# Kernel optimization log

Measured on AMD Instinct MI355X. Metric: run time of the kernel, lower is better.

## Reference

```python
import jax, jax.numpy as jnp
import numpy as np

EMBED_DIM = 2048
NUM_HEADS = 16
HEAD_DIM = EMBED_DIM // NUM_HEADS


def setup_inputs() -> dict:
    key = jax.random.key(0)
    k_x, k_qkv, k_out = jax.random.split(key, 3)
    x = jax.random.normal(k_x, (4, 2048, EMBED_DIM), dtype=jnp.float32)
    # torch nn.Linear(in, out) weight is [out, in]; y = x @ W.T
    scale = 1.0 / np.sqrt(EMBED_DIM)
    W_qkv = jax.random.uniform(k_qkv, (3 * EMBED_DIM, EMBED_DIM), dtype=jnp.float32, minval=-scale, maxval=scale)
    W_out = jax.random.uniform(k_out, (EMBED_DIM, EMBED_DIM), dtype=jnp.float32, minval=-scale, maxval=scale)
    return {"x": x, "W_qkv": W_qkv, "W_out": W_out}


def reference(x, W_qkv, W_out):
    B, T, C = x.shape
    H, D = NUM_HEADS, HEAD_DIM
    qkv = jnp.einsum("btc,fc->btf", x, W_qkv)  # [B,T,3C]
    q, k, v = jnp.split(qkv, 3, axis=-1)
    q = q.reshape(B, T, H, D).transpose(0, 2, 1, 3)  # [B,H,T,D]
    k = k.reshape(B, T, H, D).transpose(0, 2, 1, 3)
    v = v.reshape(B, T, H, D).transpose(0, 2, 1, 3)
    att = jnp.einsum("bhqd,bhkd->bhqk", q, k) / jnp.sqrt(jnp.float32(D))
    causal = jnp.tril(jnp.ones((T, T), dtype=bool))
    att = jnp.where(causal[None, None], att, -jnp.inf)
    att = jax.nn.softmax(att, axis=-1)
    out = jnp.einsum("bhqk,bhkd->bhqd", att, v)  # [B,H,T,D]
    out = out.transpose(0, 2, 1, 3).reshape(B, T, C)
    return jnp.einsum("btc,oc->bto", out, W_out)
```

## Files before the change

kernel.cpp:

```cpp
#include <hip/hip_runtime.h>
#include <hip/hip_bf16.h>
#include <math.h>

#define BDIM 4
#define TDIM 2048
#define CDIM 2048
#define HDIM 16
#define DDIM 128
#define MROWS (BDIM*TDIM)
#define NQKV (3*CDIM)
#define GK   CDIM
#define QSZ  (MROWS*CDIM)

#define NTILES 32
#define NITER  16
#define HT     8192
#define BOFF   32768

#define QSCALE 0.1275171f

typedef __attribute__((ext_vector_type(8))) short short8;
typedef __attribute__((ext_vector_type(4))) unsigned short ushort4v;
typedef __attribute__((ext_vector_type(4))) float f32x4;

__device__ __forceinline__ unsigned short f2bf(float f) {
    unsigned int u = __float_as_uint(f);
    u += 0x7fffu + ((u >> 16) & 1u);
    return (unsigned short)(u >> 16);
}

__device__ __forceinline__ void gload16(const unsigned short* g, unsigned short* l) {
    __builtin_amdgcn_global_load_lds((__attribute__((address_space(1))) void*)(g),
                                     (__attribute__((address_space(3))) void*)(l),
                                     16, 0, 0);
}

__global__ __launch_bounds__(256) void cvt_all(const float* __restrict__ x,
                                               const float* __restrict__ wqkv,
                                               const float* __restrict__ wout,
                                               unsigned short* __restrict__ xb,
                                               unsigned short* __restrict__ wqkvb,
                                               unsigned short* __restrict__ woutb)
{
    const int stride = gridDim.x * blockDim.x;
    const int t0 = blockIdx.x * blockDim.x + threadIdx.x;
    for (int i = t0; i < MROWS*CDIM/4; i += stride) {
        float4 f = ((const float4*)x)[i];
        ushort4v u;
        u[0]=f2bf(f.x); u[1]=f2bf(f.y); u[2]=f2bf(f.z); u[3]=f2bf(f.w);
        ((ushort4v*)xb)[i] = u;
    }
    for (int i = t0; i < NQKV*CDIM/4; i += stride) {
        float4 f = ((const float4*)wqkv)[i];
        const float s = (i < CDIM*CDIM/4) ? QSCALE : 1.0f;
        ushort4v u;
        u[0]=f2bf(f.x*s); u[1]=f2bf(f.y*s); u[2]=f2bf(f.z*s); u[3]=f2bf(f.w*s);
        ((ushort4v*)wqkvb)[i] = u;
    }
    for (int i = t0; i < CDIM*CDIM/4; i += stride) {
        float4 f = ((const float4*)wout)[i];
        ushort4v u;
        u[0]=f2bf(f.x); u[1]=f2bf(f.y); u[2]=f2bf(f.z); u[3]=f2bf(f.w);
        ((ushort4v*)woutb)[i] = u;
    }
}

__device__ __forceinline__ void stage_half(const unsigned short* __restrict__ T,
                                           int rowbase, int kcol,
                                           unsigned short* dst, int w, int lane)
{
    const int sw = ((lane & 3) ^ ((lane >> 3) & 3)) * 8;
#pragma unroll
    for (int j = 0; j < 2; ++j) {
        const int r = w*32 + j*16 + (lane >> 2);
        gload16(T + (size_t)(rowbase + r)*GK + kcol + sw, dst + (w*32 + j*16)*32);
    }
}

template<int MQ, int KS, int BUF, bool RDB, bool WAIT>
__device__ __forceinline__ void gphase(unsigned short* lds,
    const unsigned short* __restrict__ stT, int stRow, int stKcol, unsigned short* stDst,
    int wr, int wc, int fr, int colu, int w, int lane,
    short8 (&bfr)[4], f32x4 (&acc)[8][4])
{
    const unsigned short* Ah = lds + (BUF*2 + KS)*HT;
    const unsigned short* Bh = lds + BOFF + (BUF*2 + KS)*HT;
    short8 af[4];
#pragma unroll
    for (int mi = 0; mi < 4; ++mi)
        af[mi] = *(const short8*)&Ah[(wr*128 + (MQ*4 + mi)*16 + fr)*32 + colu];
    if (RDB) {
#pragma unroll
        for (int nj = 0; nj < 4; ++nj)
            bfr[nj] = *(const short8*)&Bh[(wc*64 + nj*16 + fr)*32 + colu];
    }
    stage_half(stT, stRow, stKcol, stDst, w, lane);
    if (WAIT) asm volatile("s_waitcnt vmcnt(4)" ::: "memory");
    __builtin_amdgcn_s_barrier();
    asm volatile("s_waitcnt lgkmcnt(0)" ::: "memory");
    __builtin_amdgcn_sched_barrier(0);
    __builtin_amdgcn_s_setprio(1);
#pragma unroll
    for (int mi = 0; mi < 4; ++mi)
#pragma unroll
        for (int nj = 0; nj < 4; ++nj)
            acc[MQ*4 + mi][nj] = __builtin_amdgcn_mfma_f32_16x16x32_bf16(af[mi], bfr[nj], acc[MQ*4 + mi][nj], 0, 0, 0);
    __builtin_amdgcn_s_setprio(0);
    __builtin_amdgcn_s_barrier();
}

template<int MODE, int RX>
__global__ __launch_bounds__(512, 2) void gemm8(const unsigned short* __restrict__ A,
                                                const unsigned short* __restrict__ B,
                                                float* __restrict__ outp,
                                                unsigned short* __restrict__ qb,
                                                unsigned short* __restrict__ kb,
                                                unsigned short* __restrict__ vt,
                                                int Nsz)
{
    extern __shared__ unsigned short lds[];
    const int tid  = threadIdx.x;
    const int w    = tid >> 6;
    const int lane = tid & 63;
    const int wr   = w >> 2, wc = w & 3;
    const int fr   = lane & 15;
    const int fg   = lane >> 4;
    const int colu = (fg ^ ((fr >> 1) & 3)) * 8;

    const int gx  = gridDim.x, gy = gridDim.y;
    const int id  = blockIdx.x + blockIdx.y * gx;
    const int xcd = id & 7;
    const int jj  = id >> 3;
    const int mx  = gx / RX;
    const int my  = (gy * RX) >> 3;
    const int bx  = (xcd % RX) * mx + (jj % mx);
    const int by  = (xcd / RX) * my + (jj / mx);
    const int m0  = bx * 256, n0 = by * 256;

    f32x4 acc[8][4];
#pragma unroll
    for (int i = 0; i < 8; ++i)
#pragma unroll
        for (int j = 0; j < 4; ++j) acc[i][j] = (f32x4)(0.f);
    short8 bfr[4];

    stage_half(A, m0, 0,  lds,             w, lane);
    stage_half(B, n0, 0,  lds + BOFF,      w, lane);
    stage_half(A, m0, 32, lds + HT,        w, lane);
    stage_half(B, n0, 32, lds + BOFF + HT, w, lane);
    stage_half(A, m0, 64, lds + 2*HT,        w, lane);
    stage_half(B, n0, 64, lds + BOFF + 2*HT, w, lane);
    asm volatile("s_waitcnt vmcnt(0)" ::: "memory");
    __builtin_amdgcn_s_barrier();

    for (int i = 0; i < NITER; ++i) {
        const int t1 = 2*i + 1;
        const int t2 = (2*i + 2 < NTILES) ? 2*i + 2 : 0;
        const int t3 = (2*i + 3 < NTILES) ? 2*i + 3 : 0;
        gphase<0,0,0,true ,false>(lds, A, m0, t1*64+32, lds + 3*HT,        wr, wc, fr, colu, w, lane, bfr, acc);
        gphase<1,0,0,false,false>(lds, B, n0, t1*64+32, lds + BOFF + 3*HT, wr, wc, fr, colu, w, lane, bfr, acc);
        gphase<0,1,0,true ,false>(lds, A, m0, t2*64,    lds,               wr, wc, fr, colu, w, lane, bfr, acc);
        gphase<1,1,0,false,true >(lds, B, n0, t2*64,    lds + BOFF,        wr, wc, fr, colu, w, lane, bfr, acc);
        gphase<0,0,1,true ,false>(lds, A, m0, t2*64+32, lds + HT,          wr, wc, fr, colu, w, lane, bfr, acc);
        gphase<1,0,1,false,false>(lds, B, n0, t2*64+32, lds + BOFF + HT,   wr, wc, fr, colu, w, lane, bfr, acc);
        gphase<0,1,1,true ,false>(lds, A, m0, t3*64,    lds + 2*HT,        wr, wc, fr, colu, w, lane, bfr, acc);
        gphase<1,1,1,false,true >(lds, B, n0, t3*64,    lds + BOFF + 2*HT, wr, wc, fr, colu, w, lane, bfr, acc);
    }
    asm volatile("s_waitcnt vmcnt(0)" ::: "memory");

    if (MODE == 0) {
#pragma unroll
        for (int mi = 0; mi < 8; ++mi)
#pragma unroll
            for (int nj = 0; nj < 4; ++nj) {
                const int n   = n0 + wc*64 + nj*16 + fr;
                const int sel = n >> 11;
                const int c   = n & 2047;
                const int hh  = c >> 7, dd = c & 127;
                const int mb  = m0 + wr*128 + mi*16 + fg*4;
                const int bb  = mb >> 11, tt = mb & 2047;
                if (sel == 2) {
                    ushort4v v;
#pragma unroll
                    for (int r = 0; r < 4; ++r) v[r] = f2bf(acc[mi][nj][r]);
                    *(ushort4v*)&vt[((size_t)(bb*HDIM + hh)*DDIM + dd)*TDIM + tt] = v;
                } else {
                    unsigned short* dstb = (sel == 0) ? qb : kb;
#pragma unroll
                    for (int r = 0; r < 4; ++r)
                        dstb[((size_t)(bb*HDIM + hh)*TDIM + tt + r)*DDIM + dd] = f2bf(acc[mi][nj][r]);
                }
            }
    } else {
#pragma unroll
        for (int mi = 0; mi < 8; ++mi)
#pragma unroll
            for (int nj = 0; nj < 4; ++nj) {
                const int n = n0 + wc*64 + nj*16 + fr;
#pragma unroll
                for (int r = 0; r < 4; ++r) {
                    const int m = m0 + wr*128 + mi*16 + fg*4 + r;
                    outp[(size_t)m*Nsz + n] = acc[mi][nj][r];
                }
            }
    }
}

__global__ __launch_bounds__(512) void attn_mfma(const unsigned short* __restrict__ Qg,
                                                 const unsigned short* __restrict__ Kg,
                                                 const unsigned short* __restrict__ Vt,
                                                 unsigned short* __restrict__ attb)
{
    extern __shared__ unsigned short smem[];
    unsigned short* KsB = smem;
    unsigned short* VsB = smem + 16384;
    unsigned short* Ps  = smem + 32768;

    const int tid  = threadIdx.x;
    const int w    = tid >> 6;
    const int lane = tid & 63;
    const int g    = lane >> 4;
    const int c    = lane & 15;
    const int bh   = blockIdx.x & 63;
    const int qb_  = 15 - (blockIdx.x >> 6);
    const int q0   = qb_ * 128;
    const int qt   = 2*qb_ + 1;
    const int qw   = q0 + w*16;

    const unsigned short* Kbh  = Kg + (size_t)bh*TDIM*DDIM;
    const unsigned short* Vtbh = Vt + (size_t)bh*DDIM*TDIM;

    short8 qf[4];
    {
        const unsigned short* qrow = Qg + ((size_t)bh*TDIM + qw + c)*DDIM + g*8;
#pragma unroll
        for (int s = 0; s < 4; ++s)
            qf[s] = *(const short8*)(qrow + s*32);
    }

    short8 onesf;
#pragma unroll
    for (int j = 0; j < 8; ++j) onesf[j] = (short)0x3F80;

    f32x4 oacc[8];
#pragma unroll
    for (int i = 0; i < 8; ++i) oacc[i] = (f32x4)(0.f);
    float m_r[4], l_r[4];
#pragma unroll
    for (int r = 0; r < 4; ++r) { m_r[r] = -INFINITY; l_r[r] = 0.f; }

#define STAGE_K(buf, kt_)                                                        \
    {                                                                            \
        _Pragma("unroll")                                                        \
        for (int j = 0; j < 2; ++j) {                                            \
            const int rw  = (w<<3) + (j<<2) + (lane >> 4);                       \
            const int sub = (lane & 15) ^ (rw & 7);                              \
            gload16(Kbh + ((size_t)((kt_)*64 + rw))*DDIM + sub*8,                \
                    &KsB[(buf)*8192 + ((w<<3) + (j<<2))*128]);                   \
        }                                                                        \
    }
#define STAGE_V(buf, kt_)                                                        \
    {                                                                            \
        _Pragma("unroll")                                                        \
        for (int j = 0; j < 2; ++j) {                                            \
            const int d   = (w<<4) + (j<<3) + (lane >> 3);                       \
            const int sub = (lane & 7) ^ (d & 7);                                \
            gload16(Vtbh + (size_t)d*TDIM + (kt_)*64 + sub*8,                    \
                    &VsB[(buf)*8192 + ((w<<4) + (j<<3))*64]);                    \
        }                                                                        \
    }

    STAGE_K(0, 0);
    STAGE_V(0, 0);
    __syncthreads();

    for (int kt = 0; kt <= qt; ++kt) {
        const int cur = kt & 1;
        if (kt < qt) { STAGE_K(cur ^ 1, kt + 1); STAGE_V(cur ^ 1, kt + 1); }

        const bool active = (kt*64) <= (qw + 15);

        if (active) {
            f32x4 sa[4];
#pragma unroll
            for (int n = 0; n < 4; ++n) sa[n] = (f32x4)(0.f);
#pragma unroll
            for (int s = 0; s < 4; ++s)
#pragma unroll
                for (int n = 0; n < 4; ++n) {
                    const int row = n*16 + c;
                    short8 bf = *(const short8*)&KsB[cur*8192 + ((row*128 + s*32 + g*8) ^ ((row&7)<<3))];
                    sa[n] = __builtin_amdgcn_mfma_f32_16x16x32_bf16(qf[s], bf, sa[n], 0, 0, 0);
                }

            if (kt*64 + 63 > qw) {
#pragma unroll
                for (int n = 0; n < 4; ++n) {
                    const int kgl = kt*64 + n*16 + c;
#pragma unroll
                    for (int r = 0; r < 4; ++r) {
                        const int qgl = qw + g*4 + r;
                        if (kgl > qgl) sa[n][r] = -INFINITY;
                    }
                }
            }

            f32x4 p[4];
            bool slow = (kt == 0);
            if (!slow) {
#pragma unroll
                for (int n = 0; n < 4; ++n)
#pragma unroll
                    for (int r = 0; r < 4; ++r)
                        p[n][r] = exp2f(sa[n][r] - m_r[r]);
                float pm = p[0][0];
#pragma unroll
                for (int n = 0; n < 4; ++n)
#pragma unroll
                    for (int r = 0; r < 4; ++r)
                        pm = fmaxf(pm, p[n][r]);
                slow = __any(pm > 256.0f);
            }
            if (slow) {
                float corr[4];
#pragma unroll
                for (int r = 0; r < 4; ++r) {
                    float mx = fmaxf(fmaxf(sa[0][r], sa[1][r]), fmaxf(sa[2][r], sa[3][r]));
                    mx = fmaxf(mx, __shfl_xor(mx, 1));
                    mx = fmaxf(mx, __shfl_xor(mx, 2));
                    mx = fmaxf(mx, __shfl_xor(mx, 4));
                    mx = fmaxf(mx, __shfl_xor(mx, 8));
                    const float mn = fmaxf(m_r[r], mx);
                    corr[r] = exp2f(m_r[r] - mn);
                    m_r[r] = mn;
                }
#pragma unroll
                for (int n = 0; n < 4; ++n)
#pragma unroll
                    for (int r = 0; r < 4; ++r)
                        p[n][r] = exp2f(sa[n][r] - m_r[r]);
#pragma unroll
                for (int i = 0; i < 8; ++i) {
                    f32x4 o = oacc[i];
                    o[0] *= corr[0]; o[1] *= corr[1]; o[2] *= corr[2]; o[3] *= corr[3];
                    oacc[i] = o;
                }
#pragma unroll
                for (int r = 0; r < 4; ++r) l_r[r] *= corr[r];
            }

            unsigned short* Pw = &Ps[w*1024];
#pragma unroll
            for (int n = 0; n < 4; ++n)
#pragma unroll
                for (int r = 0; r < 4; ++r) {
                    const int q = g*4 + r, k = n*16 + c;
                    Pw[(q*64 + k) ^ ((q&7)<<3)] = f2bf(p[n][r]);
                }
            short8 pf[2];
#pragma unroll
            for (int s2 = 0; s2 < 2; ++s2)
                pf[s2] = *(const short8*)&Pw[(c*64 + s2*32 + g*8) ^ ((c&7)<<3)];

            f32x4 rs = (f32x4)(0.f);
            rs = __builtin_amdgcn_mfma_f32_16x16x32_bf16(pf[0], onesf, rs, 0, 0, 0);
            rs = __builtin_amdgcn_mfma_f32_16x16x32_bf16(pf[1], onesf, rs, 0, 0, 0);
#pragma unroll
            for (int r = 0; r < 4; ++r) l_r[r] += rs[r];

#pragma unroll
            for (int s2 = 0; s2 < 2; ++s2)
#pragma unroll
                for (int dt = 0; dt < 8; ++dt) {
                    const int d = dt*16 + c;
                    short8 vf = *(const short8*)&VsB[cur*8192 + ((d*64 + s2*32 + g*8) ^ ((d&7)<<3))];
                    oacc[dt] = __builtin_amdgcn_mfma_f32_16x16x32_bf16(pf[s2], vf, oacc[dt], 0, 0, 0);
                }
        }

        __syncthreads();
    }

    float inv[4];
#pragma unroll
    for (int r = 0; r < 4; ++r) inv[r] = 1.f / l_r[r];
    const int b = bh >> 4, h = bh & 15;
    unsigned short* obase = attb + ((size_t)b*TDIM + qw + g*4)*CDIM + h*DDIM + c;
#pragma unroll
    for (int dt = 0; dt < 8; ++dt)
#pragma unroll
        for (int r = 0; r < 4; ++r)
            obase[(size_t)r*CDIM + dt*16] = f2bf(oacc[dt][r] * inv[r]);
}

extern "C" void kernel_launch(void* const* d_in, const int* in_sizes, int n_in,
                              void* d_out, int out_size, void* d_ws, size_t ws_size,
                              hipStream_t stream)
{
    const float* x    = (const float*)d_in[0];
    const float* Wqkv = (const float*)d_in[1];
    const float* Wout = (const float*)d_in[2];
    float* out = (float*)d_out;

    unsigned short* ws = (unsigned short*)d_ws;
    unsigned short* xb    = ws;
    unsigned short* Wqkvb = xb    + (size_t)MROWS*CDIM;
    unsigned short* Woutb = Wqkvb + (size_t)NQKV*CDIM;
    unsigned short* Qb    = Woutb + (size_t)CDIM*CDIM;
    unsigned short* Kb    = Qb + QSZ;
    unsigned short* Vtb   = Kb + QSZ;
    unsigned short* attb  = Vtb + QSZ;

    cvt_all<<<2048, 256, 0, stream>>>(x, Wqkv, Wout, xb, Wqkvb, Woutb);
    gemm8<0,4><<<dim3(MROWS/256, NQKV/256), 512, 131072, stream>>>(xb, Wqkvb, nullptr, Qb, Kb, Vtb, NQKV);
    attn_mfma<<<dim3(64*16), 512, 81920, stream>>>(Qb, Kb, Vtb, attb);
    gemm8<1,2><<<dim3(MROWS/256, CDIM/256), 512, 131072, stream>>>(attb, Woutb, out, nullptr, nullptr, nullptr, CDIM);
}
```

Baseline: 419.2 us.

## Rewrite attention with 32x32 MFMA, register-resident P, 256-row query blocks

The attention kernel switches from 16x16x32 to 32x32x16 bf16 MFMA and computes S transposed (K as the A operand), so each lane owns one query row. P is converted with packed bf16 conversion and exchanged across half-waves by shuffles instead of going through LDS, and the row sum becomes a register reduction instead of an MFMA against a ones vector. Each block now covers 256 query rows with 32 per wave, which halves the grid and drops the P scratch LDS region. The risks are higher register pressure from 16-wide accumulators, fewer blocks for load balance across the causal triangle, and the changed K swizzle having to match the read pattern.

```diff
diff --git a/kernel.cpp b/kernel.cpp
--- a/kernel.cpp
+++ b/kernel.cpp
@@ -22,11 +22,18 @@
 typedef __attribute__((ext_vector_type(8))) short short8;
 typedef __attribute__((ext_vector_type(4))) unsigned short ushort4v;
 typedef __attribute__((ext_vector_type(4))) float f32x4;
+typedef __attribute__((ext_vector_type(16))) float f32x16;
 
 __device__ __forceinline__ unsigned short f2bf(float f) {
     unsigned int u = __float_as_uint(f);
     u += 0x7fffu + ((u >> 16) & 1u);
     return (unsigned short)(u >> 16);
+}
+
+__device__ __forceinline__ unsigned int cvtpk_bf16(float lo, float hi) {
+    unsigned int r;
+    asm("v_cvt_pk_bf16_f32 %0, %1, %2" : "=v"(r) : "v"(lo), "v"(hi));
+    return r;
 }
 
 __device__ __forceinline__ void gload16(const unsigned short* g, unsigned short* l) {
@@ -214,47 +221,40 @@
     extern __shared__ unsigned short smem[];
     unsigned short* KsB = smem;
     unsigned short* VsB = smem + 16384;
-    unsigned short* Ps  = smem + 32768;
 
     const int tid  = threadIdx.x;
     const int w    = tid >> 6;
     const int lane = tid & 63;
-    const int g    = lane >> 4;
-    const int c    = lane & 15;
+    const int lq   = lane & 31;
+    const int hi   = lane >> 5;
     const int bh   = blockIdx.x & 63;
-    const int qb_  = 15 - (blockIdx.x >> 6);
-    const int q0   = qb_ * 128;
-    const int qt   = 2*qb_ + 1;
-    const int qw   = q0 + w*16;
+    const int qb_  = 7 - (blockIdx.x >> 6);
+    const int q0   = qb_ * 256;
+    const int qt   = 4*qb_ + 3;
+    const int qw   = q0 + w*32;
 
     const unsigned short* Kbh  = Kg + (size_t)bh*TDIM*DDIM;
     const unsigned short* Vtbh = Vt + (size_t)bh*DDIM*TDIM;
 
-    short8 qf[4];
+    short8 qf[8];
     {
-        const unsigned short* qrow = Qg + ((size_t)bh*TDIM + qw + c)*DDIM + g*8;
-#pragma unroll
-        for (int s = 0; s < 4; ++s)
-            qf[s] = *(const short8*)(qrow + s*32);
-    }
-
-    short8 onesf;
-#pragma unroll
-    for (int j = 0; j < 8; ++j) onesf[j] = (short)0x3F80;
-
-    f32x4 oacc[8];
-#pragma unroll
-    for (int i = 0; i < 8; ++i) oacc[i] = (f32x4)(0.f);
-    float m_r[4], l_r[4];
-#pragma unroll
-    for (int r = 0; r < 4; ++r) { m_r[r] = -INFINITY; l_r[r] = 0.f; }
+        const unsigned short* qrow = Qg + ((size_t)bh*TDIM + qw + lq)*DDIM + hi*8;
+#pragma unroll
+        for (int ds = 0; ds < 8; ++ds)
+            qf[ds] = *(const short8*)(qrow + ds*16);
+    }
+
+    f32x16 oacc[4];
+#pragma unroll
+    for (int i = 0; i < 4; ++i) oacc[i] = (f32x16)(0.f);
+    float m_r = -INFINITY, l_r = 0.f;
 
 #define STAGE_K(buf, kt_)                                                        \
     {                                                                            \
         _Pragma("unroll")                                                        \
         for (int j = 0; j < 2; ++j) {                                            \
             const int rw  = (w<<3) + (j<<2) + (lane >> 4);                       \
-            const int sub = (lane & 15) ^ (rw & 7);                              \
+            const int sub = (lane & 15) ^ (rw & 15);                             \
             gload16(Kbh + ((size_t)((kt_)*64 + rw))*DDIM + sub*8,                \
                     &KsB[(buf)*8192 + ((w<<3) + (j<<2))*128]);                   \
         }                                                                        \
@@ -278,119 +278,105 @@
         const int cur = kt & 1;
         if (kt < qt) { STAGE_K(cur ^ 1, kt + 1); STAGE_V(cur ^ 1, kt + 1); }
 
-        const bool active = (kt*64) <= (qw + 15);
-
-        if (active) {
-            f32x4 sa[4];
-#pragma unroll
-            for (int n = 0; n < 4; ++n) sa[n] = (f32x4)(0.f);
-#pragma unroll
-            for (int s = 0; s < 4; ++s)
-#pragma unroll
-                for (int n = 0; n < 4; ++n) {
-                    const int row = n*16 + c;
-                    short8 bf = *(const short8*)&KsB[cur*8192 + ((row*128 + s*32 + g*8) ^ ((row&7)<<3))];
-                    sa[n] = __builtin_amdgcn_mfma_f32_16x16x32_bf16(qf[s], bf, sa[n], 0, 0, 0);
-                }
-
-            if (kt*64 + 63 > qw) {
-#pragma unroll
-                for (int n = 0; n < 4; ++n) {
-                    const int kgl = kt*64 + n*16 + c;
-#pragma unroll
-                    for (int r = 0; r < 4; ++r) {
-                        const int qgl = qw + g*4 + r;
-                        if (kgl > qgl) sa[n][r] = -INFINITY;
+#pragma unroll
+        for (int ks2 = 0; ks2 < 2; ++ks2) {
+            const int ktb = kt*64 + ks2*32;
+            if (ktb <= qw + 31) {
+                f32x16 sa = (f32x16)(0.f);
+#pragma unroll
+                for (int ds = 0; ds < 8; ++ds) {
+                    const int kvl = ks2*32 + lq;
+                    short8 kf = *(const short8*)&KsB[cur*8192 +
+                        ((kvl*128 + ds*16 + hi*8) ^ ((kvl & 15) << 3))];
+                    sa = __builtin_amdgcn_mfma_f32_32x32x16_bf16(kf, qf[ds], sa, 0, 0, 0);
+                }
+
+                if (ktb + 31 > qw) {
+#pragma unroll
+                    for (int r = 0; r < 16; ++r) {
+                        const int kvg = ktb + (r&3) + 8*(r>>2) + 4*hi;
+                        if (kvg > qw + lq) sa[r] = -INFINITY;
                     }
                 }
+
+                float p[16];
+                bool slow = (kt == 0) && (ks2 == 0);
+                if (!slow) {
+                    float pm = 0.f;
+#pragma unroll
+                    for (int r = 0; r < 16; ++r) {
+                        p[r] = exp2f(sa[r] - m_r);
+                        pm = fmaxf(pm, p[r]);
+                    }
+                    slow = __any(pm > 256.0f);
+                }
+                if (slow) {
+                    float mx = sa[0];
+#pragma unroll
+                    for (int r = 1; r < 16; ++r) mx = fmaxf(mx, sa[r]);
+                    mx = fmaxf(mx, __shfl_xor(mx, 32));
+                    const float mn = fmaxf(m_r, mx);
+                    const float corr = exp2f(m_r - mn);
+                    m_r = mn;
+#pragma unroll
+                    for (int r = 0; r < 16; ++r) p[r] = exp2f(sa[r] - m_r);
+                    l_r *= corr;
+#pragma unroll
+                    for (int r = 0; r < 16; ++r) {
+                        const float cr = __shfl(corr, (r&3) + 8*(r>>2) + 4*hi);
+#pragma unroll
+                        for (int dt = 0; dt < 4; ++dt) oacc[dt][r] *= cr;
+                    }
+                }
+
+                float ls = 0.f;
+#pragma unroll
+                for (int r = 0; r < 16; ++r) ls += p[r];
+                l_r += ls + __shfl_xor(ls, 32);
+
+                short8 pa[2];
+#pragma unroll
+                for (int ks = 0; ks < 2; ++ks) {
+                    const unsigned int wA = cvtpk_bf16(p[8*ks+0], p[8*ks+1]);
+                    const unsigned int wB = cvtpk_bf16(p[8*ks+2], p[8*ks+3]);
+                    const unsigned int wC = cvtpk_bf16(p[8*ks+4], p[8*ks+5]);
+                    const unsigned int wD = cvtpk_bf16(p[8*ks+6], p[8*ks+7]);
+                    const unsigned int u = __shfl_xor(hi ? wA : wC, 32);
+                    const unsigned int v = __shfl_xor(hi ? wB : wD, 32);
+                    unsigned int a0 = hi ? u  : wA;
+                    unsigned int a1 = hi ? v  : wB;
+                    unsigned int a2 = hi ? wC : u;
+                    unsigned int a3 = hi ? wD : v;
+                    unsigned int aw[4] = {a0, a1, a2, a3};
+                    pa[ks] = *(short8*)aw;
+                }
+
+#pragma unroll
+                for (int ks = 0; ks < 2; ++ks)
+#pragma unroll
+                    for (int dt = 0; dt < 4; ++dt) {
+                        const int d = dt*32 + lq;
+                        short8 vf = *(const short8*)&VsB[cur*8192 +
+                            ((d*64 + ks2*32 + ks*16 + hi*8) ^ ((d & 7) << 3))];
+                        oacc[dt] = __builtin_amdgcn_mfma_f32_32x32x16_bf16(pa[ks], vf, oacc[dt], 0, 0, 0);
+                    }
             }
-
-            f32x4 p[4];
-            bool slow = (kt == 0);
-            if (!slow) {
-#pragma unroll
-                for (int n = 0; n < 4; ++n)
-#pragma unroll
-                    for (int r = 0; r < 4; ++r)
-                        p[n][r] = exp2f(sa[n][r] - m_r[r]);
-                float pm = p[0][0];
-#pragma unroll
-                for (int n = 0; n < 4; ++n)
-#pragma unroll
-                    for (int r = 0; r < 4; ++r)
-                        pm = fmaxf(pm, p[n][r]);
-                slow = __any(pm > 256.0f);
-            }
-            if (slow) {
-                float corr[4];
-#pragma unroll
-                for (int r = 0; r < 4; ++r) {
-                    float mx = fmaxf(fmaxf(sa[0][r], sa[1][r]), fmaxf(sa[2][r], sa[3][r]));
-                    mx = fmaxf(mx, __shfl_xor(mx, 1));
-                    mx = fmaxf(mx, __shfl_xor(mx, 2));
-                    mx = fmaxf(mx, __shfl_xor(mx, 4));
-                    mx = fmaxf(mx, __shfl_xor(mx, 8));
-                    const float mn = fmaxf(m_r[r], mx);
-                    corr[r] = exp2f(m_r[r] - mn);
-                    m_r[r] = mn;
-                }
-#pragma unroll
-                for (int n = 0; n < 4; ++n)
-#pragma unroll
-                    for (int r = 0; r < 4; ++r)
-                        p[n][r] = exp2f(sa[n][r] - m_r[r]);
-#pragma unroll
-                for (int i = 0; i < 8; ++i) {
-                    f32x4 o = oacc[i];
-                    o[0] *= corr[0]; o[1] *= corr[1]; o[2] *= corr[2]; o[3] *= corr[3];
-                    oacc[i] = o;
-                }
-#pragma unroll
-                for (int r = 0; r < 4; ++r) l_r[r] *= corr[r];
-            }
-
-            unsigned short* Pw = &Ps[w*1024];
-#pragma unroll
-            for (int n = 0; n < 4; ++n)
-#pragma unroll
-                for (int r = 0; r < 4; ++r) {
-                    const int q = g*4 + r, k = n*16 + c;
-                    Pw[(q*64 + k) ^ ((q&7)<<3)] = f2bf(p[n][r]);
-                }
-            short8 pf[2];
-#pragma unroll
-            for (int s2 = 0; s2 < 2; ++s2)
-                pf[s2] = *(const short8*)&Pw[(c*64 + s2*32 + g*8) ^ ((c&7)<<3)];
-
-            f32x4 rs = (f32x4)(0.f);
-            rs = __builtin_amdgcn_mfma_f32_16x16x32_bf16(pf[0], onesf, rs, 0, 0, 0);
-            rs = __builtin_amdgcn_mfma_f32_16x16x32_bf16(pf[1], onesf, rs, 0, 0, 0);
-#pragma unroll
-            for (int r = 0; r < 4; ++r) l_r[r] += rs[r];
-
-#pragma unroll
-            for (int s2 = 0; s2 < 2; ++s2)
-#pragma unroll
-                for (int dt = 0; dt < 8; ++dt) {
-                    const int d = dt*16 + c;
-                    short8 vf = *(const short8*)&VsB[cur*8192 + ((d*64 + s2*32 + g*8) ^ ((d&7)<<3))];
-                    oacc[dt] = __builtin_amdgcn_mfma_f32_16x16x32_bf16(pf[s2], vf, oacc[dt], 0, 0, 0);
-                }
         }
 
         __syncthreads();
     }
 
-    float inv[4];
-#pragma unroll
-    for (int r = 0; r < 4; ++r) inv[r] = 1.f / l_r[r];
+    const float inv = 1.f / l_r;
     const int b = bh >> 4, h = bh & 15;
-    unsigned short* obase = attb + ((size_t)b*TDIM + qw + g*4)*CDIM + h*DDIM + c;
-#pragma unroll
-    for (int dt = 0; dt < 8; ++dt)
-#pragma unroll
-        for (int r = 0; r < 4; ++r)
-            obase[(size_t)r*CDIM + dt*16] = f2bf(oacc[dt][r] * inv[r]);
+#pragma unroll
+    for (int r = 0; r < 16; ++r) {
+        const int qrw = (r&3) + 8*(r>>2) + 4*hi;
+        const float invq = __shfl(inv, qrw);
+        unsigned short* obase = attb + ((size_t)b*TDIM + qw + qrw)*CDIM + h*DDIM + lq;
+#pragma unroll
+        for (int dt = 0; dt < 4; ++dt)
+            obase[dt*32] = f2bf(oacc[dt][r] * invq);
+    }
 }
 
 extern "C" void kernel_launch(void* const* d_in, const int* in_sizes, int n_in,
@@ -413,6 +399,6 @@
 
     cvt_all<<<2048, 256, 0, stream>>>(x, Wqkv, Wout, xb, Wqkvb, Woutb);
     gemm8<0,4><<<dim3(MROWS/256, NQKV/256), 512, 131072, stream>>>(xb, Wqkvb, nullptr, Qb, Kb, Vtb, NQKV);
-    attn_mfma<<<dim3(64*16), 512, 81920, stream>>>(Qb, Kb, Vtb, attb);
+    attn_mfma<<<dim3(64*8), 512, 65536, stream>>>(Qb, Kb, Vtb, attb);
     gemm8<1,2><<<dim3(MROWS/256, CDIM/256), 512, 131072, stream>>>(attb, Woutb, out, nullptr, nullptr, nullptr, CDIM);
 }
```

Result: faster. 395.4 us (-5.7%).
